# Kernel optimization log

Hardware: AMD Instinct MI355X
Metric: run time of the kernel (lower is better)

The kernel has to match this reference:

```python
import jax, jax.numpy as jnp
import numpy as np

NEG = -1000000.0

def setup_inputs() -> dict:
    key = jax.random.key(0)
    k1, k2, k3, k4 = jax.random.split(key, 4)
    B, S, D = 32, 2048, 64  # batch_eff=batch*heads, seq_len, head_dim
    queries = jax.random.normal(k1, (B, S, D), dtype=jnp.float32)
    keys = jax.random.normal(k2, (B, S, D), dtype=jnp.float32)
    values = jax.random.normal(k3, (B, S, D), dtype=jnp.float32)
    valid_len = jax.random.randint(k4, (B,), 1, S + 1, dtype=jnp.int32)
    return {"queries": queries, "keys": keys, "values": values, "valid_len": valid_len}

def reference(queries, keys, values, valid_len):
    # scores: (B, Sq, Sk) = QK^T / sqrt(d)
    d = queries.shape[-1]
    scores = jnp.einsum('bqd,bkd->bqk', queries, keys) / jnp.sqrt(jnp.float32(d))
    # padding mask from per-batch valid key lengths: True where position is padded
    k_len = keys.shape[1]
    pad_mask = jnp.arange(k_len)[None, None, :] >= valid_len[:, None, None]  # (B,1,Sk)
    scores = jnp.where(pad_mask, NEG, scores)
    attn = jax.nn.softmax(scores, axis=-1)
    # dropout is identity in eval / reference mode
    return jnp.einsum('bqk,bkd->bqd', attn, values)
```

## Files before the change

### kernel.cpp

```cpp
#include <hip/hip_runtime.h>

typedef unsigned short ushort_t;
typedef short short8 __attribute__((ext_vector_type(8)));
typedef float f32x4 __attribute__((ext_vector_type(4)));
typedef unsigned int u32x4 __attribute__((ext_vector_type(4)));

typedef f32x4 f32x4a __attribute__((may_alias));
typedef u32x4 u32x4a __attribute__((may_alias));
typedef short8 short8a __attribute__((may_alias));

#define BC 64
#define PRP 74

#define BAR_LGKM() asm volatile("s_waitcnt lgkmcnt(0)\n\ts_barrier" ::: "memory")
#define BAR_VM8()  asm volatile("s_waitcnt vmcnt(8)\n\ts_barrier" ::: "memory")
#define BAR_VM4()  asm volatile("s_waitcnt vmcnt(4)\n\ts_barrier" ::: "memory")
#define BAR_VM0()  asm volatile("s_waitcnt vmcnt(0)\n\ts_barrier" ::: "memory")

__device__ __forceinline__ ushort_t f2bf(float x) {
    unsigned u = __float_as_uint(x);
    u = (u + 0x7fffu + ((u >> 16) & 1u)) >> 16;
    return (ushort_t)u;
}

__device__ __forceinline__ void dma16(const void* g, void* lds) {
    __builtin_amdgcn_global_load_lds(
        (const __attribute__((address_space(1))) unsigned int*)g,
        (__attribute__((address_space(3))) unsigned int*)lds, 16, 0, 0);
}

__global__ __launch_bounds__(256) void prep_kv(
    const float* __restrict__ K, const float* __restrict__ V,
    ushort_t* __restrict__ Kb, ushort_t* __restrict__ Vt,
    int* __restrict__ cnt, int S, int jtiles)
{
    __shared__ ushort_t T[64 * 66];
    const int b  = blockIdx.x / jtiles;
    const int jt = blockIdx.x % jtiles;
    const int j0 = jt * 64;
    const int tid = threadIdx.x;

    if (blockIdx.x == 0 && tid == 0) *cnt = 0;

    {
        const int jj = tid >> 2, d0 = (tid & 3) * 16;
        const float* src = K + ((size_t)b * S + j0 + jj) * 64 + d0;
        f32x4 k0 = *(const f32x4a*)(src),     k1 = *(const f32x4a*)(src + 4);
        f32x4 k2 = *(const f32x4a*)(src + 8), k3 = *(const f32x4a*)(src + 12);
        u32x4 w0, w1;
#pragma unroll
        for (int k = 0; k < 2; ++k) {
            w0[k]   = (unsigned)f2bf(k0[2*k]) | ((unsigned)f2bf(k0[2*k+1]) << 16);
            w0[k+2] = (unsigned)f2bf(k1[2*k]) | ((unsigned)f2bf(k1[2*k+1]) << 16);
            w1[k]   = (unsigned)f2bf(k2[2*k]) | ((unsigned)f2bf(k2[2*k+1]) << 16);
            w1[k+2] = (unsigned)f2bf(k3[2*k]) | ((unsigned)f2bf(k3[2*k+1]) << 16);
        }
        ushort_t* dst = Kb + ((size_t)b * S + j0 + jj) * 64 + d0;
        *(u32x4a*)dst = w0;
        *(u32x4a*)(dst + 8) = w1;
    }

    {
        const float* Vb = V + ((size_t)b * S + j0) * 64;
#pragma unroll
        for (int p = 0; p < 4; ++p) {
            int jj = p * 16 + (tid >> 4), d4 = (tid & 15) * 4;
            f32x4 v = *(const f32x4a*)(Vb + (size_t)jj * 64 + d4);
#pragma unroll
            for (int k = 0; k < 4; ++k) T[(d4 + k) * 66 + jj] = f2bf(v[k]);
        }
        __syncthreads();
        const int d = tid >> 2, j16 = (tid & 3) * 16;
        ushort_t* dst = Vt + ((size_t)(b * jtiles + jt)) * 4096 + d * 64 + j16;
        u32x4 w0, w1;
#pragma unroll
        for (int k = 0; k < 4; ++k) {
            w0[k] = (unsigned)T[d*66 + j16 + 2*k]     | ((unsigned)T[d*66 + j16 + 2*k + 1] << 16);
            w1[k] = (unsigned)T[d*66 + j16 + 8 + 2*k] | ((unsigned)T[d*66 + j16 + 9 + 2*k] << 16);
        }
        *(u32x4a*)dst = w0;
        *(u32x4a*)(dst + 8) = w1;
    }
}

__global__ __launch_bounds__(256, 3) void attn_persist(
    const float* __restrict__ Q, const ushort_t* __restrict__ Kb,
    const ushort_t* __restrict__ Vt, const int* __restrict__ VL,
    float* __restrict__ O, int* __restrict__ cnt,
    int NB, int S, int qtiles, int nitems)
{
    __shared__ __align__(16) ushort_t Kbuf[3][64 * 64];
    __shared__ __align__(16) ushort_t Vbuf[3][64 * 64];
    __shared__ int order_s[64];
    __shared__ int item_s;

    const int tid  = threadIdx.x;
    const int wave = tid >> 6;
    const int lane = tid & 63;
    const int qd   = lane >> 4;
    const int c    = lane & 15;
    const int q8   = qd * 8;

    if (tid < NB && NB <= 64) {
        const int myL = VL[tid];
        int rank = 0;
        for (int j = 0; j < NB; ++j) {
            const int Lj = VL[j];
            rank += (Lj > myL) || (Lj == myL && j < tid);
        }
        order_s[rank] = tid;
    }
    __syncthreads();

    const int r0 = wave * 16 + (lane >> 3);
    const int r1 = r0 + 8;
    const int bdp = lane & 7;
    const int swz0 = ((bdp - r0) & 7) * 16;
    const int swz1 = ((bdp - r1) & 7) * 16;
    const int ldsoff0 = wave * 1024;
    const int ldsoff1 = ldsoff0 + 512;

    const int pr0 = ((r0 >> 4) & 1) * 32 + ((r0 >> 2) & 3) * 8 + ((r0 >> 5) & 1) * 4 + (r0 & 3);
    const int pr1 = ((r1 >> 4) & 1) * 32 + ((r1 >> 2) & 3) * 8 + ((r1 >> 5) & 1) * 4 + (r1 & 3);

    int off[2][4];
#pragma unroll
    for (int x = 0; x < 2; ++x)
#pragma unroll
        for (int y = 0; y < 4; ++y) {
            const int row = y * 16 + c;
            off[x][y] = row * 128 + (((x * 4 + qd) + row) & 7) * 16;
        }

    const float qs = 0.125f * 1.4426950408889634f;
    const f32x4 zero4 = {0.0f, 0.0f, 0.0f, 0.0f};

    for (;;) {
        if (tid == 0) item_s = atomicAdd(cnt, 1);
        __syncthreads();
        const int it = item_s;
        if (it >= nitems) break;

        const int b  = order_s[it / qtiles];
        const int qt = it % qtiles;
        const int qrow0 = qt * 64 + wave * 16;
        const int L   = VL[b];
        const int nkt = (L + BC - 1) / BC;

        f32x4 qa[2], qb[2];
        {
            const float* Qb = Q + ((size_t)b * S + qrow0) * 64;
#pragma unroll
            for (int kc = 0; kc < 2; ++kc) {
                const float* qp = Qb + c * 64 + kc * 32 + q8;
                qa[kc] = *(const f32x4a*)qp;
                qb[kc] = *(const f32x4a*)(qp + 4);
            }
        }

        const char* KbB = (const char*)(Kb + (size_t)b * S * 64);
        const char* VtB = (const char*)(Vt + (size_t)b * S * 64);
        const char* kg0 = KbB + pr0 * 128 + swz0;
        const char* kg1 = KbB + pr1 * 128 + swz1;
        const char* vg0 = VtB + r0 * 128 + swz0;
        const char* vg1 = VtB + r1 * 128 + swz1;

        dma16(kg0, Kbuf[0] + ldsoff0);
        dma16(kg1, Kbuf[0] + ldsoff1);
        dma16(vg0, Vbuf[0] + ldsoff0);
        dma16(vg1, Vbuf[0] + ldsoff1);
        if (nkt > 1) {
            dma16(kg0 + 8192, Kbuf[1] + ldsoff0);
            dma16(kg1 + 8192, Kbuf[1] + ldsoff1);
            dma16(vg0 + 8192, Vbuf[1] + ldsoff0);
            dma16(vg1 + 8192, Vbuf[1] + ldsoff1);
        }

        short8 qf[2];
#pragma unroll
        for (int kc = 0; kc < 2; ++kc) {
            short8 f;
#pragma unroll
            for (int k = 0; k < 4; ++k) {
                f[k]   = (short)f2bf(qa[kc][k] * qs);
                f[k+4] = (short)f2bf(qb[kc][k] * qs);
            }
            qf[kc] = f;
        }

        f32x4 oacc[4];
#pragma unroll
        for (int dt = 0; dt < 4; ++dt) oacc[dt] = zero4;
        float rs0 = 0.0f, rs1 = 0.0f;

        int cur = 0;
        for (int kt = 0; kt < nkt; ++kt) {
            const int j0 = kt * BC;
            const ushort_t* Kt  = Kbuf[cur];
            const ushort_t* Vb_ = Vbuf[cur];

            if (kt + 2 < nkt) {
                const int pre = (cur == 0) ? 2 : cur - 1;
                const size_t ko = (size_t)(kt + 2) * 8192;
                dma16(kg0 + ko, Kbuf[pre] + ldsoff0);
                dma16(kg1 + ko, Kbuf[pre] + ldsoff1);
                dma16(vg0 + ko, Vbuf[pre] + ldsoff0);
                dma16(vg1 + ko, Vbuf[pre] + ldsoff1);
                BAR_VM8();
            } else if (kt + 1 < nkt) {
                BAR_VM4();
            } else {
                BAR_VM0();
            }

            f32x4 sacc[4];
#pragma unroll
            for (int nt = 0; nt < 4; ++nt) sacc[nt] = zero4;
            __builtin_amdgcn_s_setprio(1);
#pragma unroll
            for (int kc = 0; kc < 2; ++kc) {
#pragma unroll
                for (int nt = 0; nt < 4; ++nt) {
                    short8 kf = *(const short8a*)((const char*)Kt + off[kc][nt]);
                    sacc[nt] = __builtin_amdgcn_mfma_f32_16x16x32_bf16(kf, qf[kc], sacc[nt], 0, 0, 0);
                }
            }
            __builtin_amdgcn_s_setprio(0);

            const int lim = L - j0 - q8;
            float p[4][4];
#pragma unroll
            for (int nt = 0; nt < 4; ++nt) {
                const int kb2 = (nt & 1) * 32 + ((nt >> 1) << 2);
#pragma unroll
                for (int r = 0; r < 4; ++r) {
                    const bool valid = (kb2 + r < lim);
                    const float e = valid ? exp2f(sacc[nt][r]) : 0.0f;
                    p[nt][r] = e;
                    if (nt & 1) rs1 += e; else rs0 += e;
                }
            }

            __builtin_amdgcn_s_setprio(1);
#pragma unroll
            for (int jc = 0; jc < 2; ++jc) {
                u32x4 w;
                w[0] = (unsigned)f2bf(p[jc][0])     | ((unsigned)f2bf(p[jc][1])     << 16);
                w[1] = (unsigned)f2bf(p[jc][2])     | ((unsigned)f2bf(p[jc][3])     << 16);
                w[2] = (unsigned)f2bf(p[jc + 2][0]) | ((unsigned)f2bf(p[jc + 2][1]) << 16);
                w[3] = (unsigned)f2bf(p[jc + 2][2]) | ((unsigned)f2bf(p[jc + 2][3]) << 16);
                const short8 pf = __builtin_bit_cast(short8, w);
#pragma unroll
                for (int dt = 0; dt < 4; ++dt) {
                    short8 vf = *(const short8a*)((const char*)Vb_ + off[jc][dt]);
                    oacc[dt] = __builtin_amdgcn_mfma_f32_16x16x32_bf16(pf, vf, oacc[dt], 0, 0, 0);
                }
            }
            __builtin_amdgcn_s_setprio(0);

            BAR_LGKM();
            cur = (cur == 2) ? 0 : cur + 1;
        }

        float rsum = rs0 + rs1;
        rsum += __shfl_xor(rsum, 16);
        rsum += __shfl_xor(rsum, 32);
        const float inv = 1.0f / rsum;
#pragma unroll
        for (int r = 0; r < 4; ++r) {
            const float invr = __shfl(inv, (lane & 48) | (qd * 4 + r));
            const int row = qrow0 + qd * 4 + r;
            float* dst = O + ((size_t)b * S + row) * 64;
#pragma unroll
            for (int dt = 0; dt < 4; ++dt)
                dst[dt * 16 + c] = oacc[dt][r] * invr;
        }
    }
}

__global__ __launch_bounds__(256, 4) void attn_mono(
    const float* __restrict__ Q, const float* __restrict__ K,
    const float* __restrict__ V, const int* __restrict__ VL,
    float* __restrict__ O, int NB, int S)
{
    __shared__ ushort_t Ksh[BC * PRP];
    __shared__ ushort_t Vsh[64 * PRP];
    __shared__ ushort_t Psh[4 * 16 * PRP];
    const int tid = threadIdx.x, wave = tid >> 6, lane = tid & 63;
    const int qd = lane >> 4, c = lane & 15, q8 = qd * 8;
    const int bid = blockIdx.x;
    const int b = (bid & 7) | (((bid >> 3) & 3) << 3);
    const int qt = bid >> 5;
    const int qrow0 = qt * 64 + wave * 16;
    const int L = VL[b];
    const int nkt = (L + BC - 1) / BC;
    const size_t bbase = (size_t)b * S * 64;
    const int kj = tid >> 2, kd = (tid & 3) * 16;
    const int vp = tid & 31, vd = (tid >> 5) * 8;
    const float qs = 0.125f * 1.4426950408889634f;
    short8 qf[2];
    {
        const float* Qb = Q + bbase + (size_t)qrow0 * 64;
#pragma unroll
        for (int kc = 0; kc < 2; ++kc) {
            const float* p = Qb + c * 64 + kc * 32 + q8;
            f32x4 a = *(const f32x4a*)p;
            f32x4 bq = *(const f32x4a*)(p + 4);
            short8 f;
#pragma unroll
            for (int k = 0; k < 4; ++k) { f[k] = (short)f2bf(a[k]*qs); f[k+4] = (short)f2bf(bq[k]*qs); }
            qf[kc] = f;
        }
    }
    const f32x4 zero4 = {0.0f, 0.0f, 0.0f, 0.0f};
    f32x4 oacc[4];
#pragma unroll
    for (int dt = 0; dt < 4; ++dt) oacc[dt] = zero4;
    float lrow[4] = {0, 0, 0, 0};
    ushort_t* Pw = Psh + wave * (16 * PRP);
    for (int kt = 0; kt < nkt; ++kt) {
        const int j0 = kt * BC;
        __syncthreads();
        {
            const float* src = K + bbase + (size_t)(j0 + kj) * 64 + kd;
            f32x4 k0 = *(const f32x4a*)(src), k1 = *(const f32x4a*)(src + 4);
            f32x4 k2 = *(const f32x4a*)(src + 8), k3 = *(const f32x4a*)(src + 12);
            u32x4 w0, w1;
#pragma unroll
            for (int k = 0; k < 2; ++k) {
                w0[k]   = (unsigned)f2bf(k0[2*k]) | ((unsigned)f2bf(k0[2*k+1]) << 16);
                w0[k+2] = (unsigned)f2bf(k1[2*k]) | ((unsigned)f2bf(k1[2*k+1]) << 16);
                w1[k]   = (unsigned)f2bf(k2[2*k]) | ((unsigned)f2bf(k2[2*k+1]) << 16);
                w1[k+2] = (unsigned)f2bf(k3[2*k]) | ((unsigned)f2bf(k3[2*k+1]) << 16);
            }
            *(u32x4a*)&Ksh[kj * PRP + kd] = w0;
            *(u32x4a*)&Ksh[kj * PRP + kd + 8] = w1;
        }
        {
            const float* src = V + bbase + (size_t)(j0 + 2 * vp) * 64 + vd;
            f32x4 a0 = *(const f32x4a*)(src), a1 = *(const f32x4a*)(src + 4);
            f32x4 b0 = *(const f32x4a*)(src + 64), b1 = *(const f32x4a*)(src + 68);
#pragma unroll
            for (int kk = 0; kk < 8; ++kk) {
                float av = (kk < 4) ? a0[kk & 3] : a1[kk & 3];
                float bv = (kk < 4) ? b0[kk & 3] : b1[kk & 3];
                *(unsigned __attribute__((may_alias))*)&Vsh[(vd + kk) * PRP + 2 * vp] =
                    (unsigned)f2bf(av) | ((unsigned)f2bf(bv) << 16);
            }
        }
        __syncthreads();
        f32x4 sacc[4];
#pragma unroll
        for (int nt = 0; nt < 4; ++nt) sacc[nt] = zero4;
#pragma unroll
        for (int kc = 0; kc < 2; ++kc)
#pragma unroll
            for (int nt = 0; nt < 4; ++nt) {
                short8 kf = *(const short8a*)&Ksh[(nt * 16 + c) * PRP + kc * 32 + q8];
                sacc[nt] = __builtin_amdgcn_mfma_f32_16x16x32_bf16(qf[kc], kf, sacc[nt], 0, 0, 0);
            }
#pragma unroll
        for (int nt = 0; nt < 4; ++nt) {
            const bool valid = (j0 + nt * 16 + c) < L;
#pragma unroll
            for (int r = 0; r < 4; ++r) {
                float p = valid ? exp2f(sacc[nt][r]) : 0.0f;
                lrow[r] += p;
                Pw[(qd * 4 + r) * PRP + nt * 16 + c] = f2bf(p);
            }
        }
#pragma unroll
        for (int jc = 0; jc < 2; ++jc) {
            short8 pf = *(const short8a*)&Pw[c * PRP + jc * 32 + q8];
#pragma unroll
            for (int dt = 0; dt < 4; ++dt) {
                short8 vf = *(const short8a*)&Vsh[(dt * 16 + c) * PRP + jc * 32 + q8];
                oacc[dt] = __builtin_amdgcn_mfma_f32_16x16x32_bf16(pf, vf, oacc[dt], 0, 0, 0);
            }
        }
    }
#pragma unroll
    for (int r = 0; r < 4; ++r) {
        float ls = lrow[r];
        ls += __shfl_xor(ls, 1); ls += __shfl_xor(ls, 2);
        ls += __shfl_xor(ls, 4); ls += __shfl_xor(ls, 8);
        const float inv = 1.0f / ls;
        const int row = qrow0 + qd * 4 + r;
        float* dst = O + bbase + (size_t)row * 64;
#pragma unroll
        for (int dt = 0; dt < 4; ++dt) dst[dt * 16 + c] = oacc[dt][r] * inv;
    }
}

extern "C" void kernel_launch(void* const* d_in, const int* in_sizes, int n_in,
                              void* d_out, int out_size, void* d_ws, size_t ws_size,
                              hipStream_t stream) {
    const float* Q = (const float*)d_in[0];
    const float* K = (const float*)d_in[1];
    const float* V = (const float*)d_in[2];
    const int*  VL = (const int*)d_in[3];
    float*      Op = (float*)d_out;

    const int NB = in_sizes[3];
    const int S  = in_sizes[0] / (NB * 64);
    const int qtiles = S / 64;
    const int jtiles = S / 64;
    const size_t nelem = (size_t)NB * S * 64;
    const size_t bf_bytes = nelem * 2;

    if (ws_size >= 256 + 2 * bf_bytes && NB <= 64) {
        int* cnt = (int*)d_ws;
        ushort_t* Kb = (ushort_t*)((char*)d_ws + 256);
        ushort_t* Vt = (ushort_t*)((char*)d_ws + 256 + bf_bytes);
        prep_kv<<<dim3(NB * jtiles), dim3(256), 0, stream>>>(K, V, Kb, Vt, cnt, S, jtiles);
        const int nitems = NB * qtiles;
        const int grid = nitems < 768 ? nitems : 768;
        attn_persist<<<dim3(grid), dim3(256), 0, stream>>>(
            Q, Kb, Vt, VL, Op, cnt, NB, S, qtiles, nitems);
    } else {
        attn_mono<<<dim3(NB * qtiles), dim3(256), 0, stream>>>(Q, K, V, VL, Op, NB, S);
    }
}
```

Baseline: 153.9 us.

## Process two query tiles per work item and deepen K/V prefetch to four stages

Each persistent block now claims two adjacent 64-row query tiles per atomic fetch and reuses every K/V tile loaded into LDS for both, halving LDS fill traffic and global K/V reads per query row. The pipeline grows from three to four buffers, prefetching three tiles ahead. Occupancy drops from 3 to 2 blocks per CU and the grid from 768 to 512, with more registers per wave for the doubled accumulators. The persistent path now also requires an even number of query tiles.

```diff
diff --git a/kernel.cpp b/kernel.cpp
--- a/kernel.cpp
+++ b/kernel.cpp
@@ -13,6 +13,7 @@
 #define PRP 74
 
 #define BAR_LGKM() asm volatile("s_waitcnt lgkmcnt(0)\n\ts_barrier" ::: "memory")
+#define BAR_VM12() asm volatile("s_waitcnt vmcnt(12)\n\ts_barrier" ::: "memory")
 #define BAR_VM8()  asm volatile("s_waitcnt vmcnt(8)\n\ts_barrier" ::: "memory")
 #define BAR_VM4()  asm volatile("s_waitcnt vmcnt(4)\n\ts_barrier" ::: "memory")
 #define BAR_VM0()  asm volatile("s_waitcnt vmcnt(0)\n\ts_barrier" ::: "memory")
@@ -83,14 +84,14 @@
     }
 }
 
-__global__ __launch_bounds__(256, 3) void attn_persist(
+__global__ __launch_bounds__(256, 2) void attn_persist(
     const float* __restrict__ Q, const ushort_t* __restrict__ Kb,
     const ushort_t* __restrict__ Vt, const int* __restrict__ VL,
     float* __restrict__ O, int* __restrict__ cnt,
     int NB, int S, int qtiles, int nitems)
 {
-    __shared__ __align__(16) ushort_t Kbuf[3][64 * 64];
-    __shared__ __align__(16) ushort_t Vbuf[3][64 * 64];
+    __shared__ __align__(16) ushort_t Kbuf[4][64 * 64];
+    __shared__ __align__(16) ushort_t Vbuf[4][64 * 64];
     __shared__ int order_s[64];
     __shared__ int item_s;
 
@@ -136,34 +137,39 @@
     const f32x4 zero4 = {0.0f, 0.0f, 0.0f, 0.0f};
 
     for (;;) {
-        if (tid == 0) item_s = atomicAdd(cnt, 1);
+        if (tid == 0) item_s = atomicAdd(cnt, 2);
         __syncthreads();
         const int it = item_s;
         if (it >= nitems) break;
 
-        const int b  = order_s[it / qtiles];
-        const int qt = it % qtiles;
-        const int qrow0 = qt * 64 + wave * 16;
+        const int b   = order_s[it / qtiles];
+        const int qtA = it % qtiles;
+        const int qrow0A = qtA * 64 + wave * 16;
+        const int qrow0B = qrow0A + 64;
         const int L   = VL[b];
         const int nkt = (L + BC - 1) / BC;
 
-        f32x4 qa[2], qb[2];
+        f32x4 qaA[2], qbA[2], qaB[2], qbB[2];
         {
-            const float* Qb = Q + ((size_t)b * S + qrow0) * 64;
+            const float* QbA = Q + ((size_t)b * S + qrow0A) * 64;
+            const float* QbB = Q + ((size_t)b * S + qrow0B) * 64;
 #pragma unroll
             for (int kc = 0; kc < 2; ++kc) {
-                const float* qp = Qb + c * 64 + kc * 32 + q8;
-                qa[kc] = *(const f32x4a*)qp;
-                qb[kc] = *(const f32x4a*)(qp + 4);
-            }
-        }
-
-        const char* KbB = (const char*)(Kb + (size_t)b * S * 64);
-        const char* VtB = (const char*)(Vt + (size_t)b * S * 64);
-        const char* kg0 = KbB + pr0 * 128 + swz0;
-        const char* kg1 = KbB + pr1 * 128 + swz1;
-        const char* vg0 = VtB + r0 * 128 + swz0;
-        const char* vg1 = VtB + r1 * 128 + swz1;
+                const float* pA = QbA + c * 64 + kc * 32 + q8;
+                const float* pB = QbB + c * 64 + kc * 32 + q8;
+                qaA[kc] = *(const f32x4a*)pA;
+                qbA[kc] = *(const f32x4a*)(pA + 4);
+                qaB[kc] = *(const f32x4a*)pB;
+                qbB[kc] = *(const f32x4a*)(pB + 4);
+            }
+        }
+
+        const char* KbB_ = (const char*)(Kb + (size_t)b * S * 64);
+        const char* VtB_ = (const char*)(Vt + (size_t)b * S * 64);
+        const char* kg0 = KbB_ + pr0 * 128 + swz0;
+        const char* kg1 = KbB_ + pr1 * 128 + swz1;
+        const char* vg0 = VtB_ + r0 * 128 + swz0;
+        const char* vg1 = VtB_ + r1 * 128 + swz1;
 
         dma16(kg0, Kbuf[0] + ldsoff0);
         dma16(kg1, Kbuf[0] + ldsoff1);
@@ -175,37 +181,47 @@
             dma16(vg0 + 8192, Vbuf[1] + ldsoff0);
             dma16(vg1 + 8192, Vbuf[1] + ldsoff1);
         }
-
-        short8 qf[2];
+        if (nkt > 2) {
+            dma16(kg0 + 16384, Kbuf[2] + ldsoff0);
+            dma16(kg1 + 16384, Kbuf[2] + ldsoff1);
+            dma16(vg0 + 16384, Vbuf[2] + ldsoff0);
+            dma16(vg1 + 16384, Vbuf[2] + ldsoff1);
+        }
+
+        short8 qfA[2], qfB[2];
 #pragma unroll
         for (int kc = 0; kc < 2; ++kc) {
-            short8 f;
+            short8 fA, fB;
 #pragma unroll
             for (int k = 0; k < 4; ++k) {
-                f[k]   = (short)f2bf(qa[kc][k] * qs);
-                f[k+4] = (short)f2bf(qb[kc][k] * qs);
-            }
-            qf[kc] = f;
-        }
-
-        f32x4 oacc[4];
-#pragma unroll
-        for (int dt = 0; dt < 4; ++dt) oacc[dt] = zero4;
-        float rs0 = 0.0f, rs1 = 0.0f;
-
-        int cur = 0;
+                fA[k]   = (short)f2bf(qaA[kc][k] * qs);
+                fA[k+4] = (short)f2bf(qbA[kc][k] * qs);
+                fB[k]   = (short)f2bf(qaB[kc][k] * qs);
+                fB[k+4] = (short)f2bf(qbB[kc][k] * qs);
+            }
+            qfA[kc] = fA;
+            qfB[kc] = fB;
+        }
+
+        f32x4 oaccA[4], oaccB[4];
+#pragma unroll
+        for (int dt = 0; dt < 4; ++dt) { oaccA[dt] = zero4; oaccB[dt] = zero4; }
+        float rsA0 = 0.0f, rsA1 = 0.0f, rsB0 = 0.0f, rsB1 = 0.0f;
+
         for (int kt = 0; kt < nkt; ++kt) {
             const int j0 = kt * BC;
-            const ushort_t* Kt  = Kbuf[cur];
-            const ushort_t* Vb_ = Vbuf[cur];
-
-            if (kt + 2 < nkt) {
-                const int pre = (cur == 0) ? 2 : cur - 1;
-                const size_t ko = (size_t)(kt + 2) * 8192;
+            const ushort_t* Kt  = Kbuf[kt & 3];
+            const ushort_t* Vb_ = Vbuf[kt & 3];
+
+            if (kt + 3 < nkt) {
+                const int pre = (kt + 3) & 3;
+                const size_t ko = (size_t)(kt + 3) * 8192;
                 dma16(kg0 + ko, Kbuf[pre] + ldsoff0);
                 dma16(kg1 + ko, Kbuf[pre] + ldsoff1);
                 dma16(vg0 + ko, Vbuf[pre] + ldsoff0);
                 dma16(vg1 + ko, Vbuf[pre] + ldsoff1);
+                BAR_VM12();
+            } else if (kt + 2 < nkt) {
                 BAR_VM8();
             } else if (kt + 1 < nkt) {
                 BAR_VM4();
@@ -213,67 +229,132 @@
                 BAR_VM0();
             }
 
-            f32x4 sacc[4];
-#pragma unroll
-            for (int nt = 0; nt < 4; ++nt) sacc[nt] = zero4;
-            __builtin_amdgcn_s_setprio(1);
-#pragma unroll
-            for (int kc = 0; kc < 2; ++kc) {
+            const int lim = L - j0 - q8;
+
+            {
+                f32x4 sacc[4];
+#pragma unroll
+                for (int nt = 0; nt < 4; ++nt) sacc[nt] = zero4;
+                __builtin_amdgcn_s_setprio(1);
+#pragma unroll
+                for (int kc = 0; kc < 2; ++kc) {
+#pragma unroll
+                    for (int nt = 0; nt < 4; ++nt) {
+                        short8 kf = *(const short8a*)((const char*)Kt + off[kc][nt]);
+                        sacc[nt] = __builtin_amdgcn_mfma_f32_16x16x32_bf16(kf, qfA[kc], sacc[nt], 0, 0, 0);
+                    }
+                }
+                __builtin_amdgcn_s_setprio(0);
+
+                float p[4][4];
 #pragma unroll
                 for (int nt = 0; nt < 4; ++nt) {
-                    short8 kf = *(const short8a*)((const char*)Kt + off[kc][nt]);
-                    sacc[nt] = __builtin_amdgcn_mfma_f32_16x16x32_bf16(kf, qf[kc], sacc[nt], 0, 0, 0);
+                    const int kb2 = (nt & 1) * 32 + ((nt >> 1) << 2);
+#pragma unroll
+                    for (int r = 0; r < 4; ++r) {
+                        const bool valid = (kb2 + r < lim);
+                        const float e = valid ? exp2f(sacc[nt][r]) : 0.0f;
+                        p[nt][r] = e;
+                        if (nt & 1) rsA1 += e; else rsA0 += e;
+                    }
                 }
-            }
-            __builtin_amdgcn_s_setprio(0);
-
-            const int lim = L - j0 - q8;
-            float p[4][4];
-#pragma unroll
-            for (int nt = 0; nt < 4; ++nt) {
-                const int kb2 = (nt & 1) * 32 + ((nt >> 1) << 2);
-#pragma unroll
-                for (int r = 0; r < 4; ++r) {
-                    const bool valid = (kb2 + r < lim);
-                    const float e = valid ? exp2f(sacc[nt][r]) : 0.0f;
-                    p[nt][r] = e;
-                    if (nt & 1) rs1 += e; else rs0 += e;
+
+                __builtin_amdgcn_s_setprio(1);
+#pragma unroll
+                for (int jc = 0; jc < 2; ++jc) {
+                    u32x4 w;
+                    w[0] = (unsigned)f2bf(p[jc][0])     | ((unsigned)f2bf(p[jc][1])     << 16);
+                    w[1] = (unsigned)f2bf(p[jc][2])     | ((unsigned)f2bf(p[jc][3])     << 16);
+                    w[2] = (unsigned)f2bf(p[jc + 2][0]) | ((unsigned)f2bf(p[jc + 2][1]) << 16);
+                    w[3] = (unsigned)f2bf(p[jc + 2][2]) | ((unsigned)f2bf(p[jc + 2][3]) << 16);
+                    const short8 pf = __builtin_bit_cast(short8, w);
+#pragma unroll
+                    for (int dt = 0; dt < 4; ++dt) {
+                        short8 vf = *(const short8a*)((const char*)Vb_ + off[jc][dt]);
+                        oaccA[dt] = __builtin_amdgcn_mfma_f32_16x16x32_bf16(pf, vf, oaccA[dt], 0, 0, 0);
+                    }
                 }
-            }
-
-            __builtin_amdgcn_s_setprio(1);
-#pragma unroll
-            for (int jc = 0; jc < 2; ++jc) {
-                u32x4 w;
-                w[0] = (unsigned)f2bf(p[jc][0])     | ((unsigned)f2bf(p[jc][1])     << 16);
-                w[1] = (unsigned)f2bf(p[jc][2])     | ((unsigned)f2bf(p[jc][3])     << 16);
-                w[2] = (unsigned)f2bf(p[jc + 2][0]) | ((unsigned)f2bf(p[jc + 2][1]) << 16);
-                w[3] = (unsigned)f2bf(p[jc + 2][2]) | ((unsigned)f2bf(p[jc + 2][3]) << 16);
-                const short8 pf = __builtin_bit_cast(short8, w);
-#pragma unroll
-                for (int dt = 0; dt < 4; ++dt) {
-                    short8 vf = *(const short8a*)((const char*)Vb_ + off[jc][dt]);
-                    oacc[dt] = __builtin_amdgcn_mfma_f32_16x16x32_bf16(pf, vf, oacc[dt], 0, 0, 0);
+                __builtin_amdgcn_s_setprio(0);
+            }
+
+            {
+                f32x4 sacc[4];
+#pragma unroll
+                for (int nt = 0; nt < 4; ++nt) sacc[nt] = zero4;
+                __builtin_amdgcn_s_setprio(1);
+#pragma unroll
+                for (int kc = 0; kc < 2; ++kc) {
+#pragma unroll
+                    for (int nt = 0; nt < 4; ++nt) {
+                        short8 kf = *(const short8a*)((const char*)Kt + off[kc][nt]);
+                        sacc[nt] = __builtin_amdgcn_mfma_f32_16x16x32_bf16(kf, qfB[kc], sacc[nt], 0, 0, 0);
+                    }
                 }
-            }
-            __builtin_amdgcn_s_setprio(0);
+                __builtin_amdgcn_s_setprio(0);
+
+                float p[4][4];
+#pragma unroll
+                for (int nt = 0; nt < 4; ++nt) {
+                    const int kb2 = (nt & 1) * 32 + ((nt >> 1) << 2);
+#pragma unroll
+                    for (int r = 0; r < 4; ++r) {
+                        const bool valid = (kb2 + r < lim);
+                        const float e = valid ? exp2f(sacc[nt][r]) : 0.0f;
+                        p[nt][r] = e;
+                        if (nt & 1) rsB1 += e; else rsB0 += e;
+                    }
+                }
+
+                __builtin_amdgcn_s_setprio(1);
+#pragma unroll
+                for (int jc = 0; jc < 2; ++jc) {
+                    u32x4 w;
+                    w[0] = (unsigned)f2bf(p[jc][0])     | ((unsigned)f2bf(p[jc][1])     << 16);
+                    w[1] = (unsigned)f2bf(p[jc][2])     | ((unsigned)f2bf(p[jc][3])     << 16);
+                    w[2] = (unsigned)f2bf(p[jc + 2][0]) | ((unsigned)f2bf(p[jc + 2][1]) << 16);
+                    w[3] = (unsigned)f2bf(p[jc + 2][2]) | ((unsigned)f2bf(p[jc + 2][3]) << 16);
+                    const short8 pf = __builtin_bit_cast(short8, w);
+#pragma unroll
+                    for (int dt = 0; dt < 4; ++dt) {
+                        short8 vf = *(const short8a*)((const char*)Vb_ + off[jc][dt]);
+                        oaccB[dt] = __builtin_amdgcn_mfma_f32_16x16x32_bf16(pf, vf, oaccB[dt], 0, 0, 0);
+                    }
+                }
+                __builtin_amdgcn_s_setprio(0);
+            }
 
             BAR_LGKM();
-            cur = (cur == 2) ? 0 : cur + 1;
-        }
-
-        float rsum = rs0 + rs1;
-        rsum += __shfl_xor(rsum, 16);
-        rsum += __shfl_xor(rsum, 32);
-        const float inv = 1.0f / rsum;
-#pragma unroll
-        for (int r = 0; r < 4; ++r) {
-            const float invr = __shfl(inv, (lane & 48) | (qd * 4 + r));
-            const int row = qrow0 + qd * 4 + r;
-            float* dst = O + ((size_t)b * S + row) * 64;
-#pragma unroll
-            for (int dt = 0; dt < 4; ++dt)
-                dst[dt * 16 + c] = oacc[dt][r] * invr;
+        }
+
+        {
+            float rsum = rsA0 + rsA1;
+            rsum += __shfl_xor(rsum, 16);
+            rsum += __shfl_xor(rsum, 32);
+            const float inv = 1.0f / rsum;
+#pragma unroll
+            for (int r = 0; r < 4; ++r) {
+                const float invr = __shfl(inv, (lane & 48) | (qd * 4 + r));
+                const int row = qrow0A + qd * 4 + r;
+                float* dst = O + ((size_t)b * S + row) * 64;
+#pragma unroll
+                for (int dt = 0; dt < 4; ++dt)
+                    dst[dt * 16 + c] = oaccA[dt][r] * invr;
+            }
+        }
+        {
+            float rsum = rsB0 + rsB1;
+            rsum += __shfl_xor(rsum, 16);
+            rsum += __shfl_xor(rsum, 32);
+            const float inv = 1.0f / rsum;
+#pragma unroll
+            for (int r = 0; r < 4; ++r) {
+                const float invr = __shfl(inv, (lane & 48) | (qd * 4 + r));
+                const int row = qrow0B + qd * 4 + r;
+                float* dst = O + ((size_t)b * S + row) * 64;
+#pragma unroll
+                for (int dt = 0; dt < 4; ++dt)
+                    dst[dt * 16 + c] = oaccB[dt][r] * invr;
+            }
         }
     }
 }
@@ -408,13 +489,14 @@
     const size_t nelem = (size_t)NB * S * 64;
     const size_t bf_bytes = nelem * 2;
 
-    if (ws_size >= 256 + 2 * bf_bytes && NB <= 64) {
+    if (ws_size >= 256 + 2 * bf_bytes && NB <= 64 && (qtiles % 2) == 0) {
         int* cnt = (int*)d_ws;
         ushort_t* Kb = (ushort_t*)((char*)d_ws + 256);
         ushort_t* Vt = (ushort_t*)((char*)d_ws + 256 + bf_bytes);
         prep_kv<<<dim3(NB * jtiles), dim3(256), 0, stream>>>(K, V, Kb, Vt, cnt, S, jtiles);
         const int nitems = NB * qtiles;
-        const int grid = nitems < 768 ? nitems : 768;
+        const int npairs = nitems / 2;
+        const int grid = npairs < 512 ? npairs : 512;
         attn_persist<<<dim3(grid), dim3(256), 0, stream>>>(
             Q, Kb, Vt, VL, Op, cnt, NB, S, qtiles, nitems);
     } else {
```

New measurement: 167.7 us. +9.0%, slower.

## Split work queue into per-XCD groups with snake batch assignment, cheaper bf16 pack

Applied to the files above, without the earlier changes.

Work items now come from eight atomic counters, one per block group (blockIdx mod 8, which lines up with the XCDs). Batches, sorted by valid length, are dealt to the groups in a snake order so each group gets similar load and its K/V traffic stays in one L2. This cuts atomic contention and cross-XCD cache sharing, at the risk of load imbalance because groups cannot steal work from each other. Separately, the P-to-bf16 packing switches from round-to-nearest-even to a simpler add-0x8000 rounding with fewer ALU ops, and the grid is fixed at 768 blocks.

```diff
diff --git a/kernel.cpp b/kernel.cpp
--- a/kernel.cpp
+++ b/kernel.cpp
@@ -40,7 +40,7 @@
     const int j0 = jt * 64;
     const int tid = threadIdx.x;
 
-    if (blockIdx.x == 0 && tid == 0) *cnt = 0;
+    if (blockIdx.x == 0 && tid < 8) cnt[tid] = 0;
 
     {
         const int jj = tid >> 2, d0 = (tid & 3) * 16;
@@ -87,7 +87,7 @@
     const float* __restrict__ Q, const ushort_t* __restrict__ Kb,
     const ushort_t* __restrict__ Vt, const int* __restrict__ VL,
     float* __restrict__ O, int* __restrict__ cnt,
-    int NB, int S, int qtiles, int nitems)
+    int NB, int S, int qtiles)
 {
     __shared__ __align__(16) ushort_t Kbuf[3][64 * 64];
     __shared__ __align__(16) ushort_t Vbuf[3][64 * 64];
@@ -100,6 +100,11 @@
     const int qd   = lane >> 4;
     const int c    = lane & 15;
     const int q8   = qd * 8;
+
+    const int ngrp = (NB >= 8 && (NB % 8) == 0) ? 8 : 1;
+    const int bpg  = NB / ngrp;
+    const int ipg  = bpg * qtiles;
+    const int g    = blockIdx.x % ngrp;
 
     if (tid < NB && NB <= 64) {
         const int myL = VL[tid];
@@ -136,13 +141,15 @@
     const f32x4 zero4 = {0.0f, 0.0f, 0.0f, 0.0f};
 
     for (;;) {
-        if (tid == 0) item_s = atomicAdd(cnt, 1);
+        if (tid == 0) item_s = atomicAdd(cnt + g, 1);
         __syncthreads();
         const int it = item_s;
-        if (it >= nitems) break;
-
-        const int b  = order_s[it / qtiles];
+        if (it >= ipg) break;
+
+        const int kb = it / qtiles;
         const int qt = it % qtiles;
+        const int rank = kb * ngrp + ((kb & 1) ? (ngrp - 1 - g) : g);
+        const int b  = order_s[rank];
         const int qrow0 = qt * 64 + wave * 16;
         const int L   = VL[b];
         const int nkt = (L + BC - 1) / BC;
@@ -245,10 +252,16 @@
 #pragma unroll
             for (int jc = 0; jc < 2; ++jc) {
                 u32x4 w;
-                w[0] = (unsigned)f2bf(p[jc][0])     | ((unsigned)f2bf(p[jc][1])     << 16);
-                w[1] = (unsigned)f2bf(p[jc][2])     | ((unsigned)f2bf(p[jc][3])     << 16);
-                w[2] = (unsigned)f2bf(p[jc + 2][0]) | ((unsigned)f2bf(p[jc + 2][1]) << 16);
-                w[3] = (unsigned)f2bf(p[jc + 2][2]) | ((unsigned)f2bf(p[jc + 2][3]) << 16);
+#pragma unroll
+                for (int h = 0; h < 2; ++h) {
+                    const float* pp = p[jc + 2 * h];
+                    unsigned u0 = __float_as_uint(pp[0]) + 0x8000u;
+                    unsigned u1 = __float_as_uint(pp[1]) + 0x8000u;
+                    unsigned u2 = __float_as_uint(pp[2]) + 0x8000u;
+                    unsigned u3 = __float_as_uint(pp[3]) + 0x8000u;
+                    w[2*h]   = (u0 >> 16) | (u1 & 0xffff0000u);
+                    w[2*h+1] = (u2 >> 16) | (u3 & 0xffff0000u);
+                }
                 const short8 pf = __builtin_bit_cast(short8, w);
 #pragma unroll
                 for (int dt = 0; dt < 4; ++dt) {
@@ -413,10 +426,8 @@
         ushort_t* Kb = (ushort_t*)((char*)d_ws + 256);
         ushort_t* Vt = (ushort_t*)((char*)d_ws + 256 + bf_bytes);
         prep_kv<<<dim3(NB * jtiles), dim3(256), 0, stream>>>(K, V, Kb, Vt, cnt, S, jtiles);
-        const int nitems = NB * qtiles;
-        const int grid = nitems < 768 ? nitems : 768;
-        attn_persist<<<dim3(grid), dim3(256), 0, stream>>>(
-            Q, Kb, Vt, VL, Op, cnt, NB, S, qtiles, nitems);
+        attn_persist<<<dim3(768), dim3(256), 0, stream>>>(
+            Q, Kb, Vt, VL, Op, cnt, NB, S, qtiles);
     } else {
         attn_mono<<<dim3(NB * qtiles), dim3(256), 0, stream>>>(Q, K, V, VL, Op, NB, S);
     }
```

Result: no change. 152.1 us (-1.1%).
